# Kernel tuning notes

Hardware: AMD Instinct MI355X
Metric: run time of the kernel (lower is better)

The kernel has to match this reference:

```python
import jax, jax.numpy as jnp
import numpy as np

INPUT_SIZE = 32
HIDDEN_SIZE = 64
OUTPUT_SIZE = 8
B, T = 8192, 128


def setup_inputs() -> dict:
    key = jax.random.key(0)
    ks = jax.random.split(key, 7)
    s_ih = 1.0 / np.sqrt(HIDDEN_SIZE)
    return {
        "x": jax.random.normal(ks[0], (B, T, INPUT_SIZE), dtype=jnp.float32),
        "W_ih": jax.random.uniform(ks[1], (4 * HIDDEN_SIZE, INPUT_SIZE), minval=-s_ih, maxval=s_ih),
        "W_hh": jax.random.uniform(ks[2], (4 * HIDDEN_SIZE, HIDDEN_SIZE), minval=-s_ih, maxval=s_ih),
        "b_ih": jax.random.uniform(ks[3], (4 * HIDDEN_SIZE,), minval=-s_ih, maxval=s_ih),
        "b_hh": jax.random.uniform(ks[4], (4 * HIDDEN_SIZE,), minval=-s_ih, maxval=s_ih),
        "W_fc": jax.random.uniform(ks[5], (OUTPUT_SIZE, HIDDEN_SIZE), minval=-s_ih, maxval=s_ih),
        "b_fc": jax.random.uniform(ks[6], (OUTPUT_SIZE,), minval=-s_ih, maxval=s_ih),
    }


def _lstm_last_h(x, W_ih, W_hh, b_ih, b_hh):
    Bc, Tc, _ = x.shape
    H = HIDDEN_SIZE
    # Precompute the input contribution to all gates once: [B, T, 4H]
    x_gates = jnp.einsum("bti,gi->btg", x, W_ih) + b_ih + b_hh

    def step(carry, xg_t):  # xg_t: [B, 4H]
        h, c = carry
        gates = xg_t + h @ W_hh.T
        i = jax.nn.sigmoid(gates[:, 0 * H:1 * H])
        f = jax.nn.sigmoid(gates[:, 1 * H:2 * H])
        g = jnp.tanh(gates[:, 2 * H:3 * H])
        o = jax.nn.sigmoid(gates[:, 3 * H:4 * H])
        c = f * c + i * g
        h = o * jnp.tanh(c)
        return (h, c), None

    h0 = jnp.zeros((Bc, H), dtype=x.dtype)
    c0 = jnp.zeros((Bc, H), dtype=x.dtype)
    (h_T, _), _ = jax.lax.scan(step, (h0, c0), jnp.swapaxes(x_gates, 0, 1))
    return h_T  # [B, H] = out[:, -1, :]


def reference(x, W_ih, W_hh, b_ih, b_hh, W_fc, b_fc):
    h_last = _lstm_last_h(x, W_ih, W_hh, b_ih, b_hh)
    return h_last @ W_fc.T + b_fc  # [B, OUTPUT_SIZE]
```

## Files before the change

kernel.cpp:

```cpp
#include <hip/hip_runtime.h>
#include <stdint.h>


#define T_STEPS 128
#define ISZ 32
#define HSZ 64
#define B_TOT 8192
#define B_TILE 16
#define T_CHUNK 32
#define HPAD 144

typedef short bf16x8 __attribute__((ext_vector_type(8)));
typedef float f32x4 __attribute__((ext_vector_type(4)));

#define LOG2E 1.44269504088896340736f

__device__ __forceinline__ float bf2f(unsigned short s) {
    union { unsigned int u; float f; } v; v.u = ((unsigned int)s) << 16; return v.f;
}
__device__ __forceinline__ unsigned short f2bf(float f) {
    union { float f; unsigned int u; } v; v.f = f;
    unsigned int u = v.u;
    return (unsigned short)((u + 0x7fffu + ((u >> 16) & 1u)) >> 16);
}
__device__ __forceinline__ float sigf(float x) {
    return __builtin_amdgcn_rcpf(1.0f + __builtin_amdgcn_exp2f(-LOG2E * x));
}
__device__ __forceinline__ float tanh_fast(float x) {
    return 1.0f - 2.0f * __builtin_amdgcn_rcpf(1.0f + __builtin_amdgcn_exp2f((2.0f * LOG2E) * x));
}

template <bool F32>
__device__ __forceinline__ float ldin(const void* p, size_t i) {
    if (F32) return ((const float*)p)[i];
    return bf2f(((const unsigned short*)p)[i]);
}

template <bool F32>
__device__ __forceinline__ void run_body(
    const void* xv, const void* Wihv, const void* Whhv, const void* bihv,
    const void* bhhv, const void* Wfcv, const void* bfcv, void* outv,
    unsigned short (&hbuf)[2][B_TILE][HPAD],
    unsigned short (&xbuf)[T_CHUNK][B_TILE][40],
    float (&hfin)[B_TILE][HSZ + 4])
{
    const int tid  = threadIdx.x;
    const int wid  = tid >> 6;
    const int lane = tid & 63;
    const int q    = lane >> 4;
    const int tn   = lane & 15;
    const int u    = wid * 16 + tn;
    const int b0   = blockIdx.x * B_TILE;

    bf16x8 wf[4][3];
    f32x4 biasC[4];
    #pragma unroll
    for (int g = 0; g < 4; ++g) {
        const int row = g * HSZ + u;
        #pragma unroll
        for (int j = 0; j < 8; ++j) {
            wf[g][0][j] = (short)f2bf(ldin<F32>(Whhv, row * HSZ + q * 8 + j));
            wf[g][1][j] = (short)f2bf(ldin<F32>(Whhv, row * HSZ + 32 + q * 8 + j));
            wf[g][2][j] = (short)f2bf(ldin<F32>(Wihv, row * ISZ + q * 8 + j));
        }
        const float b = ldin<F32>(bihv, row) + ldin<F32>(bhhv, row);
        #pragma unroll
        for (int e = 0; e < 4; ++e) biasC[g][e] = b;
    }

    for (int i = tid; i < 2 * B_TILE * HPAD; i += 256) ((unsigned short*)hbuf)[i] = 0;

    float cst[4] = {0.f, 0.f, 0.f, 0.f};
    float hl[4]  = {0.f, 0.f, 0.f, 0.f};
    f32x4 accx[4];

    for (int tc = 0; tc < T_STEPS / T_CHUNK; ++tc) {
        if (F32) {
            const float* xf = (const float*)xv;
            for (int idx = tid; idx < B_TILE * T_CHUNK * 4; idx += 256) {
                const int m  = idx >> 7;
                const int rm = idx & 127;
                const int tl = rm >> 2;
                const int ch = rm & 3;
                const size_t base = ((size_t)(b0 + m) * T_STEPS + (tc * T_CHUNK + tl)) * ISZ + ch * 8;
                const f32x4 v0 = *(const f32x4*)(xf + base);
                const f32x4 v1 = *(const f32x4*)(xf + base + 4);
                bf16x8 w;
                #pragma unroll
                for (int j = 0; j < 4; ++j) {
                    w[j]     = (short)f2bf(v0[j]);
                    w[4 + j] = (short)f2bf(v1[j]);
                }
                *(bf16x8*)&xbuf[tl][m][ch * 8] = w;
            }
        } else {
            const unsigned short* xu = (const unsigned short*)xv;
            for (int idx = tid; idx < B_TILE * T_CHUNK * 4; idx += 256) {
                const int m  = idx >> 7;
                const int rm = idx & 127;
                const int tl = rm >> 2;
                const int ch = rm & 3;
                const uint4 v = *(const uint4*)(xu + ((size_t)(b0 + m) * T_STEPS + (tc * T_CHUNK + tl)) * ISZ + ch * 8);
                *(uint4*)&xbuf[tl][m][ch * 8] = v;
            }
        }
        __syncthreads();

        {
            const bf16x8 ax = *(const bf16x8*)&xbuf[0][tn][q * 8];
            #pragma unroll
            for (int g = 0; g < 4; ++g)
                accx[g] = __builtin_amdgcn_mfma_f32_16x16x32_bf16(ax, wf[g][2], biasC[g], 0, 0, 0);
        }

        #pragma unroll 2
        for (int tl = 0; tl < T_CHUNK; ++tl) {
            const int t  = tc * T_CHUNK + tl;
            const int rb = t & 1, wb = rb ^ 1;
            const bf16x8 a0  = *(const bf16x8*)&hbuf[rb][tn][q * 8];
            const bf16x8 a1  = *(const bf16x8*)&hbuf[rb][tn][32 + q * 8];
            const bf16x8 ax2 = *(const bf16x8*)&xbuf[(tl + 1) & (T_CHUNK - 1)][tn][q * 8];

            f32x4 acc[4];
            #pragma unroll
            for (int g = 0; g < 4; ++g)
                acc[g] = __builtin_amdgcn_mfma_f32_16x16x32_bf16(a0, wf[g][0], accx[g], 0, 0, 0);
            #pragma unroll
            for (int g = 0; g < 4; ++g)
                acc[g] = __builtin_amdgcn_mfma_f32_16x16x32_bf16(a1, wf[g][1], acc[g], 0, 0, 0);

            #pragma unroll
            for (int r = 0; r < 4; ++r) {
                const float gi = sigf(acc[0][r]);
                const float gf = sigf(acc[1][r]);
                const float gg = tanh_fast(acc[2][r]);
                const float go = sigf(acc[3][r]);
                cst[r] = gf * cst[r] + gi * gg;
                const float hv = go * tanh_fast(cst[r]);
                hl[r] = hv;
                const int m = q * 4 + r;
                hbuf[wb][m][u] = f2bf(hv);
            }

            #pragma unroll
            for (int g = 0; g < 4; ++g)
                accx[g] = __builtin_amdgcn_mfma_f32_16x16x32_bf16(ax2, wf[g][2], biasC[g], 0, 0, 0);

            __syncthreads();
        }
    }

    #pragma unroll
    for (int r = 0; r < 4; ++r) hfin[q * 4 + r][u] = hl[r];
    __syncthreads();
    if (tid < B_TILE * 8) {
        const int m = tid >> 3, j = tid & 7;
        float s = ldin<F32>(bfcv, j);
        #pragma unroll
        for (int k = 0; k < HSZ; ++k) s += hfin[m][k] * ldin<F32>(Wfcv, j * HSZ + k);
        const size_t o = (size_t)(b0 + m) * 8 + j;
        if (F32) ((float*)outv)[o] = s;
        else     ((unsigned short*)outv)[o] = f2bf(s);
    }
}

__global__ __launch_bounds__(256, 2) void lstm_fused(
    const void* __restrict__ x, const void* __restrict__ Wih,
    const void* __restrict__ Whh, const void* __restrict__ bih,
    const void* __restrict__ bhh, const void* __restrict__ Wfc,
    const void* __restrict__ bfc, void* __restrict__ out)
{
    __shared__ unsigned short hbuf[2][B_TILE][HPAD];
    __shared__ unsigned short xbuf[T_CHUNK][B_TILE][40];
    __shared__ float hfin[B_TILE][HSZ + 4];

    const unsigned short* xu = (const unsigned short*)x;
    const int lane = threadIdx.x & 63;
    const unsigned short s0 = xu[lane * 2];
    const unsigned short s1 = xu[lane * 2 + 1];
    const int big = (((s0 >> 7) & 0xFF) >= 0x90) || (((s1 >> 7) & 0xFF) >= 0x90);
    const bool isf32 = __any(big) != 0;

    if (isf32) run_body<true >(x, Wih, Whh, bih, bhh, Wfc, bfc, out, hbuf, xbuf, hfin);
    else       run_body<false>(x, Wih, Whh, bih, bhh, Wfc, bfc, out, hbuf, xbuf, hfin);
}

extern "C" void kernel_launch(void* const* d_in, const int* in_sizes, int n_in,
                              void* d_out, int out_size, void* d_ws, size_t ws_size,
                              hipStream_t stream) {
    lstm_fused<<<dim3(B_TOT / B_TILE), dim3(256), 0, stream>>>(
        d_in[0], d_in[1], d_in[2], d_in[3], d_in[4], d_in[5], d_in[6], d_out);
}
```

Baseline: 273.6 us.

## Halve batch tile to 8 rows per block, padding MFMA rows for more blocks

Each block now handles 8 batch rows instead of 16. It still issues 16-row MFMAs, using a permuted row mapping (jx) so that only the first two accumulator rows per lane hold real sequences, and only those get the gate math. The grid doubles and launch bounds ask for 4 blocks per CU, trading half-wasted MFMA work for more concurrent blocks to hide the serial recurrence latency. hbuf keeps 16 rows, and the rows that are never written stay zero.

```diff
diff --git a/kernel.cpp b/kernel.cpp
--- a/kernel.cpp
+++ b/kernel.cpp
@@ -6,7 +6,8 @@
 #define ISZ 32
 #define HSZ 64
 #define B_TOT 8192
-#define B_TILE 16
+#define B_TILE 8
+#define BROWS 16
 #define T_CHUNK 32
 #define HPAD 144
 
@@ -40,7 +41,7 @@
 __device__ __forceinline__ void run_body(
     const void* xv, const void* Wihv, const void* Whhv, const void* bihv,
     const void* bhhv, const void* Wfcv, const void* bfcv, void* outv,
-    unsigned short (&hbuf)[2][B_TILE][HPAD],
+    unsigned short (&hbuf)[2][BROWS][HPAD],
     unsigned short (&xbuf)[T_CHUNK][B_TILE][40],
     float (&hfin)[B_TILE][HSZ + 4])
 {
@@ -51,6 +52,7 @@
     const int tn   = lane & 15;
     const int u    = wid * 16 + tn;
     const int b0   = blockIdx.x * B_TILE;
+    const int jx   = ((tn >> 2) << 1) | (tn & 1);
 
     bf16x8 wf[4][3];
     f32x4 biasC[4];
@@ -68,10 +70,10 @@
         for (int e = 0; e < 4; ++e) biasC[g][e] = b;
     }
 
-    for (int i = tid; i < 2 * B_TILE * HPAD; i += 256) ((unsigned short*)hbuf)[i] = 0;
+    for (int i = tid; i < 2 * BROWS * HPAD; i += 256) ((unsigned short*)hbuf)[i] = 0;
 
-    float cst[4] = {0.f, 0.f, 0.f, 0.f};
-    float hl[4]  = {0.f, 0.f, 0.f, 0.f};
+    float cst[2] = {0.f, 0.f};
+    float hl[2]  = {0.f, 0.f};
     f32x4 accx[4];
 
     for (int tc = 0; tc < T_STEPS / T_CHUNK; ++tc) {
@@ -107,7 +109,7 @@
         __syncthreads();
 
         {
-            const bf16x8 ax = *(const bf16x8*)&xbuf[0][tn][q * 8];
+            const bf16x8 ax = *(const bf16x8*)&xbuf[0][jx][q * 8];
             #pragma unroll
             for (int g = 0; g < 4; ++g)
                 accx[g] = __builtin_amdgcn_mfma_f32_16x16x32_bf16(ax, wf[g][2], biasC[g], 0, 0, 0);
@@ -119,7 +121,7 @@
             const int rb = t & 1, wb = rb ^ 1;
             const bf16x8 a0  = *(const bf16x8*)&hbuf[rb][tn][q * 8];
             const bf16x8 a1  = *(const bf16x8*)&hbuf[rb][tn][32 + q * 8];
-            const bf16x8 ax2 = *(const bf16x8*)&xbuf[(tl + 1) & (T_CHUNK - 1)][tn][q * 8];
+            const bf16x8 ax2 = *(const bf16x8*)&xbuf[(tl + 1) & (T_CHUNK - 1)][jx][q * 8];
 
             f32x4 acc[4];
             #pragma unroll
@@ -130,15 +132,15 @@
                 acc[g] = __builtin_amdgcn_mfma_f32_16x16x32_bf16(a1, wf[g][1], acc[g], 0, 0, 0);
 
             #pragma unroll
-            for (int r = 0; r < 4; ++r) {
-                const float gi = sigf(acc[0][r]);
-                const float gf = sigf(acc[1][r]);
-                const float gg = tanh_fast(acc[2][r]);
-                const float go = sigf(acc[3][r]);
-                cst[r] = gf * cst[r] + gi * gg;
-                const float hv = go * tanh_fast(cst[r]);
-                hl[r] = hv;
-                const int m = q * 4 + r;
+            for (int rr = 0; rr < 2; ++rr) {
+                const float gi = sigf(acc[0][rr]);
+                const float gf = sigf(acc[1][rr]);
+                const float gg = tanh_fast(acc[2][rr]);
+                const float go = sigf(acc[3][rr]);
+                cst[rr] = gf * cst[rr] + gi * gg;
+                const float hv = go * tanh_fast(cst[rr]);
+                hl[rr] = hv;
+                const int m = q * 4 + rr;
                 hbuf[wb][m][u] = f2bf(hv);
             }
 
@@ -151,7 +153,7 @@
     }
 
     #pragma unroll
-    for (int r = 0; r < 4; ++r) hfin[q * 4 + r][u] = hl[r];
+    for (int rr = 0; rr < 2; ++rr) hfin[q * 2 + rr][u] = hl[rr];
     __syncthreads();
     if (tid < B_TILE * 8) {
         const int m = tid >> 3, j = tid & 7;
@@ -164,13 +166,13 @@
     }
 }
 
-__global__ __launch_bounds__(256, 2) void lstm_fused(
+__global__ __launch_bounds__(256, 4) void lstm_fused(
     const void* __restrict__ x, const void* __restrict__ Wih,
     const void* __restrict__ Whh, const void* __restrict__ bih,
     const void* __restrict__ bhh, const void* __restrict__ Wfc,
     const void* __restrict__ bfc, void* __restrict__ out)
 {
-    __shared__ unsigned short hbuf[2][B_TILE][HPAD];
+    __shared__ unsigned short hbuf[2][BROWS][HPAD];
     __shared__ unsigned short xbuf[T_CHUNK][B_TILE][40];
     __shared__ float hfin[B_TILE][HSZ + 4];
 
```

Measured after the change: 285.0 us. 1.04x slower.

## Process two 16-row batch sub-tiles per block to interleave independent recurrences

Applied to the files above, without the earlier changes.

Each block now handles 32 batch rows as two independent 16-row halves. Every wave issues MFMAs and gate math for both halves in each timestep, so two independent dependency chains interleave and one barrier per step is shared between them. The time chunk is halved to keep x staging in LDS bounded, hfin is aliased onto hbuf, and launch bounds drop to one block per CU. In exchange the grid halves to 256 blocks and register pressure rises, which could leave CUs underused on a 256-CU part.

```diff
diff --git a/kernel.cpp b/kernel.cpp
--- a/kernel.cpp
+++ b/kernel.cpp
@@ -6,8 +6,8 @@
 #define ISZ 32
 #define HSZ 64
 #define B_TOT 8192
-#define B_TILE 16
-#define T_CHUNK 32
+#define B_TILE 32
+#define T_CHUNK 16
 #define HPAD 144
 
 typedef short bf16x8 __attribute__((ext_vector_type(8)));
@@ -41,8 +41,7 @@
     const void* xv, const void* Wihv, const void* Whhv, const void* bihv,
     const void* bhhv, const void* Wfcv, const void* bfcv, void* outv,
     unsigned short (&hbuf)[2][B_TILE][HPAD],
-    unsigned short (&xbuf)[T_CHUNK][B_TILE][40],
-    float (&hfin)[B_TILE][HSZ + 4])
+    unsigned short (&xbuf)[T_CHUNK][B_TILE][40])
 {
     const int tid  = threadIdx.x;
     const int wid  = tid >> 6;
@@ -70,16 +69,18 @@
 
     for (int i = tid; i < 2 * B_TILE * HPAD; i += 256) ((unsigned short*)hbuf)[i] = 0;
 
-    float cst[4] = {0.f, 0.f, 0.f, 0.f};
-    float hl[4]  = {0.f, 0.f, 0.f, 0.f};
-    f32x4 accx[4];
+    float cstA[4] = {0.f, 0.f, 0.f, 0.f};
+    float cstB[4] = {0.f, 0.f, 0.f, 0.f};
+    float hlA[4]  = {0.f, 0.f, 0.f, 0.f};
+    float hlB[4]  = {0.f, 0.f, 0.f, 0.f};
+    f32x4 accxA[4], accxB[4];
 
     for (int tc = 0; tc < T_STEPS / T_CHUNK; ++tc) {
         if (F32) {
             const float* xf = (const float*)xv;
             for (int idx = tid; idx < B_TILE * T_CHUNK * 4; idx += 256) {
-                const int m  = idx >> 7;
-                const int rm = idx & 127;
+                const int m  = idx >> 6;
+                const int rm = idx & 63;
                 const int tl = rm >> 2;
                 const int ch = rm & 3;
                 const size_t base = ((size_t)(b0 + m) * T_STEPS + (tc * T_CHUNK + tl)) * ISZ + ch * 8;
@@ -96,8 +97,8 @@
         } else {
             const unsigned short* xu = (const unsigned short*)xv;
             for (int idx = tid; idx < B_TILE * T_CHUNK * 4; idx += 256) {
-                const int m  = idx >> 7;
-                const int rm = idx & 127;
+                const int m  = idx >> 6;
+                const int rm = idx & 63;
                 const int tl = rm >> 2;
                 const int ch = rm & 3;
                 const uint4 v = *(const uint4*)(xu + ((size_t)(b0 + m) * T_STEPS + (tc * T_CHUNK + tl)) * ISZ + ch * 8);
@@ -107,53 +108,83 @@
         __syncthreads();
 
         {
-            const bf16x8 ax = *(const bf16x8*)&xbuf[0][tn][q * 8];
-            #pragma unroll
-            for (int g = 0; g < 4; ++g)
-                accx[g] = __builtin_amdgcn_mfma_f32_16x16x32_bf16(ax, wf[g][2], biasC[g], 0, 0, 0);
-        }
-
-        #pragma unroll 2
+            const bf16x8 axA = *(const bf16x8*)&xbuf[0][tn][q * 8];
+            const bf16x8 axB = *(const bf16x8*)&xbuf[0][16 + tn][q * 8];
+            #pragma unroll
+            for (int g = 0; g < 4; ++g)
+                accxA[g] = __builtin_amdgcn_mfma_f32_16x16x32_bf16(axA, wf[g][2], biasC[g], 0, 0, 0);
+            #pragma unroll
+            for (int g = 0; g < 4; ++g)
+                accxB[g] = __builtin_amdgcn_mfma_f32_16x16x32_bf16(axB, wf[g][2], biasC[g], 0, 0, 0);
+        }
+
         for (int tl = 0; tl < T_CHUNK; ++tl) {
             const int t  = tc * T_CHUNK + tl;
             const int rb = t & 1, wb = rb ^ 1;
-            const bf16x8 a0  = *(const bf16x8*)&hbuf[rb][tn][q * 8];
-            const bf16x8 a1  = *(const bf16x8*)&hbuf[rb][tn][32 + q * 8];
-            const bf16x8 ax2 = *(const bf16x8*)&xbuf[(tl + 1) & (T_CHUNK - 1)][tn][q * 8];
-
-            f32x4 acc[4];
-            #pragma unroll
-            for (int g = 0; g < 4; ++g)
-                acc[g] = __builtin_amdgcn_mfma_f32_16x16x32_bf16(a0, wf[g][0], accx[g], 0, 0, 0);
-            #pragma unroll
-            for (int g = 0; g < 4; ++g)
-                acc[g] = __builtin_amdgcn_mfma_f32_16x16x32_bf16(a1, wf[g][1], acc[g], 0, 0, 0);
+            const int nt = (tl + 1) & (T_CHUNK - 1);
+            const bf16x8 aA0  = *(const bf16x8*)&hbuf[rb][tn][q * 8];
+            const bf16x8 aA1  = *(const bf16x8*)&hbuf[rb][tn][32 + q * 8];
+            const bf16x8 aB0  = *(const bf16x8*)&hbuf[rb][16 + tn][q * 8];
+            const bf16x8 aB1  = *(const bf16x8*)&hbuf[rb][16 + tn][32 + q * 8];
+            const bf16x8 axA2 = *(const bf16x8*)&xbuf[nt][tn][q * 8];
+            const bf16x8 axB2 = *(const bf16x8*)&xbuf[nt][16 + tn][q * 8];
+
+            f32x4 accA[4], accB[4];
+            #pragma unroll
+            for (int g = 0; g < 4; ++g)
+                accA[g] = __builtin_amdgcn_mfma_f32_16x16x32_bf16(aA0, wf[g][0], accxA[g], 0, 0, 0);
+            #pragma unroll
+            for (int g = 0; g < 4; ++g)
+                accB[g] = __builtin_amdgcn_mfma_f32_16x16x32_bf16(aB0, wf[g][0], accxB[g], 0, 0, 0);
+            #pragma unroll
+            for (int g = 0; g < 4; ++g)
+                accA[g] = __builtin_amdgcn_mfma_f32_16x16x32_bf16(aA1, wf[g][1], accA[g], 0, 0, 0);
+            #pragma unroll
+            for (int g = 0; g < 4; ++g)
+                accB[g] = __builtin_amdgcn_mfma_f32_16x16x32_bf16(aB1, wf[g][1], accB[g], 0, 0, 0);
 
             #pragma unroll
             for (int r = 0; r < 4; ++r) {
-                const float gi = sigf(acc[0][r]);
-                const float gf = sigf(acc[1][r]);
-                const float gg = tanh_fast(acc[2][r]);
-                const float go = sigf(acc[3][r]);
-                cst[r] = gf * cst[r] + gi * gg;
-                const float hv = go * tanh_fast(cst[r]);
-                hl[r] = hv;
-                const int m = q * 4 + r;
-                hbuf[wb][m][u] = f2bf(hv);
-            }
-
-            #pragma unroll
-            for (int g = 0; g < 4; ++g)
-                accx[g] = __builtin_amdgcn_mfma_f32_16x16x32_bf16(ax2, wf[g][2], biasC[g], 0, 0, 0);
+                const float gi = sigf(accA[0][r]);
+                const float gf = sigf(accA[1][r]);
+                const float gg = tanh_fast(accA[2][r]);
+                const float go = sigf(accA[3][r]);
+                cstA[r] = gf * cstA[r] + gi * gg;
+                const float hv = go * tanh_fast(cstA[r]);
+                hlA[r] = hv;
+                hbuf[wb][q * 4 + r][u] = f2bf(hv);
+            }
+            #pragma unroll
+            for (int r = 0; r < 4; ++r) {
+                const float gi = sigf(accB[0][r]);
+                const float gf = sigf(accB[1][r]);
+                const float gg = tanh_fast(accB[2][r]);
+                const float go = sigf(accB[3][r]);
+                cstB[r] = gf * cstB[r] + gi * gg;
+                const float hv = go * tanh_fast(cstB[r]);
+                hlB[r] = hv;
+                hbuf[wb][16 + q * 4 + r][u] = f2bf(hv);
+            }
+
+            #pragma unroll
+            for (int g = 0; g < 4; ++g)
+                accxA[g] = __builtin_amdgcn_mfma_f32_16x16x32_bf16(axA2, wf[g][2], biasC[g], 0, 0, 0);
+            #pragma unroll
+            for (int g = 0; g < 4; ++g)
+                accxB[g] = __builtin_amdgcn_mfma_f32_16x16x32_bf16(axB2, wf[g][2], biasC[g], 0, 0, 0);
 
             __syncthreads();
         }
     }
 
+    float (*hfin)[HSZ + 4] = reinterpret_cast<float (*)[HSZ + 4]>(&hbuf[0][0][0]);
     #pragma unroll
-    for (int r = 0; r < 4; ++r) hfin[q * 4 + r][u] = hl[r];
+    for (int r = 0; r < 4; ++r) {
+        hfin[q * 4 + r][u]      = hlA[r];
+        hfin[16 + q * 4 + r][u] = hlB[r];
+    }
     __syncthreads();
-    if (tid < B_TILE * 8) {
+    {
         const int m = tid >> 3, j = tid & 7;
         float s = ldin<F32>(bfcv, j);
         #pragma unroll
@@ -164,15 +195,14 @@
     }
 }
 
-__global__ __launch_bounds__(256, 2) void lstm_fused(
+__global__ __launch_bounds__(256, 1) void lstm_fused(
     const void* __restrict__ x, const void* __restrict__ Wih,
     const void* __restrict__ Whh, const void* __restrict__ bih,
     const void* __restrict__ bhh, const void* __restrict__ Wfc,
     const void* __restrict__ bfc, void* __restrict__ out)
 {
-    __shared__ unsigned short hbuf[2][B_TILE][HPAD];
-    __shared__ unsigned short xbuf[T_CHUNK][B_TILE][40];
-    __shared__ float hfin[B_TILE][HSZ + 4];
+    __shared__ __align__(16) unsigned short hbuf[2][B_TILE][HPAD];
+    __shared__ __align__(16) unsigned short xbuf[T_CHUNK][B_TILE][40];
 
     const unsigned short* xu = (const unsigned short*)x;
     const int lane = threadIdx.x & 63;
@@ -181,8 +211,8 @@
     const int big = (((s0 >> 7) & 0xFF) >= 0x90) || (((s1 >> 7) & 0xFF) >= 0x90);
     const bool isf32 = __any(big) != 0;
 
-    if (isf32) run_body<true >(x, Wih, Whh, bih, bhh, Wfc, bfc, out, hbuf, xbuf, hfin);
-    else       run_body<false>(x, Wih, Whh, bih, bhh, Wfc, bfc, out, hbuf, xbuf, hfin);
+    if (isf32) run_body<true >(x, Wih, Whh, bih, bhh, Wfc, bfc, out, hbuf, xbuf);
+    else       run_body<false>(x, Wih, Whh, bih, bhh, Wfc, bfc, out, hbuf, xbuf);
 }
 
 extern "C" void kernel_launch(void* const* d_in, const int* in_sizes, int n_in,
```

Result: slower. 321.0 us (+17.3%).
